# Kernel optimization log

Measured on AMD Instinct MI355X. Metric: run time of the kernel, lower is better.

Reference implementation:

```python
import jax, jax.numpy as jnp
import numpy as np

N, E, DIN, H, D = 100000, 1600000, 256, 4, 32  # nodes, edges, in_feats, heads, out_feats
NEG_SLOPE = 0.2


def setup_inputs() -> dict:
    key = jax.random.key(0)
    ks = jax.random.split(key, 6)
    feat = jax.random.normal(ks[0], (N, DIN), jnp.float32)
    src = jax.random.randint(ks[1], (E,), 0, N, jnp.int32)
    dst = jax.random.randint(ks[2], (E,), 0, N, jnp.int32)
    # fc weight, xavier-normal-ish scale
    W = jax.random.normal(ks[3], (H * D, DIN), jnp.float32) * (2.0 / (DIN + H * D)) ** 0.5
    attn_l = jax.random.normal(ks[4], (1, H, D), jnp.float32) * 0.1
    attn_r = jax.random.normal(ks[5], (1, H, D), jnp.float32) * 0.1
    bias = jnp.zeros((H * D,), jnp.float32)
    return dict(feat=feat, src=src, dst=dst, W=W, attn_l=attn_l, attn_r=attn_r, bias=bias)


def reference(feat, src, dst, W, attn_l, attn_r, bias):
    n = feat.shape[0]
    # node projection: [N, H, D]
    ft = (feat @ W.T).reshape(n, H, D)
    # per-node attention logits: [N, H]
    el = jnp.sum(ft * attn_l, axis=-1)
    er = jnp.sum(ft * attn_r, axis=-1)
    # edge scores (u_add_v + LeakyReLU): [E, H]
    e = jax.nn.leaky_relu(el[src] + er[dst], NEG_SLOPE)
    # segment softmax over incoming edges of each dst node
    m = jax.ops.segment_max(e, dst, num_segments=n)
    m = jnp.where(jnp.isfinite(m), m, 0.0)  # guard zero-in-degree nodes
    ae = jnp.exp(e - m[dst])
    denom = jax.ops.segment_sum(ae, dst, num_segments=n)
    a = ae / denom[dst]  # [E, H]
    # weighted scatter-aggregate (u_mul_e + sum): [N, H, D]
    out = jax.ops.segment_sum(ft[src] * a[:, :, None], dst, num_segments=n)
    return out + bias.reshape(1, H, D)
```

## Files before the change

### kernel.cpp

```cpp
#include <hip/hip_runtime.h>
#include <hip/hip_bf16.h>


#define DIN 256
#define HD 128
#define NEG_SLOPE 0.2f
#define BUCKW 1024
#define BINE 4096
#define CAP  18432

typedef float f32x4 __attribute__((ext_vector_type(4)));
typedef short s16x8 __attribute__((ext_vector_type(8)));

static __device__ __forceinline__ unsigned short f2bf(float x) {
    unsigned u = __float_as_uint(x);
    unsigned r = (u + 0x7FFFu + ((u >> 16) & 1u)) >> 16;
    return (unsigned short)r;
}
static __device__ __forceinline__ uint pk2(float a, float b) {
    return (uint)f2bf(a) | ((uint)f2bf(b) << 16);
}

__global__ void transw_kernel(const float* __restrict__ W, unsigned short* __restrict__ Wtb) {
    int idx = blockIdx.x * blockDim.x + threadIdx.x;
    if (idx >= HD * DIN) return;
    int i = idx & 7, c = (idx >> 3) & 127, kb = idx >> 10;
    Wtb[idx] = f2bf(W[(size_t)c * DIN + kb * 8 + i]);
}

__global__ __launch_bounds__(256, 4) void gemm_kernel(
    const float* __restrict__ feat, const unsigned short* __restrict__ Wtb,
    unsigned short* __restrict__ ftu, const float* __restrict__ attn_l,
    const float* __restrict__ attn_r, float* __restrict__ el,
    float* __restrict__ er, int n)
{
    const int tid = threadIdx.x;
    const int lane = tid & 63;
    const int wv = tid >> 6;
    const int l16 = lane & 15, lq = lane >> 4;
    const int row0 = (int)blockIdx.x * 128 + wv * 32;

    f32x4 acc[2][8] = {};
    const int ar0 = row0 + l16, ar1 = row0 + 16 + l16;
    const bool ok0 = ar0 < n, ok1 = ar1 < n;
    const float* fp0 = feat + (size_t)ar0 * DIN;
    const float* fp1 = feat + (size_t)ar1 * DIN;
#pragma unroll
    for (int kc = 0; kc < 4; ++kc) {
#pragma unroll
        for (int kk = 0; kk < 2; ++kk) {
            const int koff = kc * 64 + kk * 32 + lq * 8;
            union { s16x8 v; uint w[4]; } a0, a1;
            a0.v = (s16x8)(short)0;
            a1.v = (s16x8)(short)0;
            if (ok0) {
                float4 fa = *(const float4*)(fp0 + koff);
                float4 fb = *(const float4*)(fp0 + koff + 4);
                a0.w[0] = pk2(fa.x, fa.y); a0.w[1] = pk2(fa.z, fa.w);
                a0.w[2] = pk2(fb.x, fb.y); a0.w[3] = pk2(fb.z, fb.w);
            }
            if (ok1) {
                float4 fa = *(const float4*)(fp1 + koff);
                float4 fb = *(const float4*)(fp1 + koff + 4);
                a1.w[0] = pk2(fa.x, fa.y); a1.w[1] = pk2(fa.z, fa.w);
                a1.w[2] = pk2(fb.x, fb.y); a1.w[3] = pk2(fb.z, fb.w);
            }
            const int kb = kc * 8 + kk * 4 + lq;
            const unsigned short* bp = Wtb + ((size_t)kb * 128 + l16) * 8;
#pragma unroll
            for (int n4 = 0; n4 < 8; ++n4) {
                s16x8 b = *(const s16x8*)(bp + n4 * 128);
                acc[0][n4] = __builtin_amdgcn_mfma_f32_16x16x32_bf16(a0.v, b, acc[0][n4], 0, 0, 0);
                acc[1][n4] = __builtin_amdgcn_mfma_f32_16x16x32_bf16(a1.v, b, acc[1][n4], 0, 0, 0);
            }
        }
    }

    float al8[8], ar8[8];
#pragma unroll
    for (int n4 = 0; n4 < 8; ++n4) {
        al8[n4] = attn_l[n4 * 16 + l16];
        ar8[n4] = attn_r[n4 * 16 + l16];
    }
#pragma unroll
    for (int m = 0; m < 2; ++m) {
#pragma unroll
        for (int n4 = 0; n4 < 8; ++n4)
#pragma unroll
            for (int j = 0; j < 4; ++j) {
                int r = row0 + m * 16 + lq * 4 + j;
                if (r < n) ftu[(size_t)r * HD + n4 * 16 + l16] = f2bf(acc[m][n4][j]);
            }
#pragma unroll
        for (int j = 0; j < 4; ++j) {
            const int r = row0 + m * 16 + lq * 4 + j;
#pragma unroll
            for (int h = 0; h < 4; ++h) {
                float sl = acc[m][2 * h][j] * al8[2 * h] + acc[m][2 * h + 1][j] * al8[2 * h + 1];
                float sr = acc[m][2 * h][j] * ar8[2 * h] + acc[m][2 * h + 1][j] * ar8[2 * h + 1];
#pragma unroll
                for (int off = 1; off < 16; off <<= 1) {
                    sl += __shfl_xor(sl, off);
                    sr += __shfl_xor(sr, off);
                }
                if (l16 == ((j << 2) | h) && r < n) {
                    el[r * 4 + h] = sl;
                    er[r * 4 + h] = sr;
                }
            }
        }
    }
}

__global__ __launch_bounds__(512) void bin_kernel(
    const int* __restrict__ src, const int* __restrict__ dst,
    int* __restrict__ gcur, int* __restrict__ esrc,
    unsigned short* __restrict__ edlo, int e)
{
    __shared__ int h[128], lb[128], gb[128], sc[128];
    __shared__ int tot;
    __shared__ int ps[BINE];
    __shared__ unsigned short pd[BINE];
    __shared__ unsigned char pb[BINE];
    const int tid = threadIdx.x;
    if (tid < 128) h[tid] = 0;
    __syncthreads();
    const int base = blockIdx.x * BINE + tid * 8;
    int sv[8], dv[8], rk[8];
    const int cnt = min(8, max(0, e - base));
    if (cnt == 8) {
        *(int4*)&sv[0] = *(const int4*)&src[base];
        *(int4*)&sv[4] = *(const int4*)&src[base + 4];
        *(int4*)&dv[0] = *(const int4*)&dst[base];
        *(int4*)&dv[4] = *(const int4*)&dst[base + 4];
    } else {
        for (int m = 0; m < cnt; ++m) { sv[m] = src[base + m]; dv[m] = dst[base + m]; }
    }
    for (int m = 0; m < cnt; ++m)
        rk[m] = atomicAdd(&h[dv[m] >> 10], 1);
    __syncthreads();
    if (tid < 128) sc[tid] = h[tid];
    __syncthreads();
    for (int off = 1; off < 128; off <<= 1) {
        int v = (tid < 128 && tid >= off) ? sc[tid - off] : 0;
        __syncthreads();
        if (tid < 128) sc[tid] += v;
        __syncthreads();
    }
    if (tid < 128) {
        lb[tid] = sc[tid] - h[tid];
        if (h[tid] > 0) gb[tid] = atomicAdd(&gcur[tid], h[tid]);
    }
    if (tid == 127) tot = sc[127];
    __syncthreads();
    for (int m = 0; m < cnt; ++m) {
        int b = dv[m] >> 10;
        int pos = lb[b] + rk[m];
        ps[pos] = sv[m];
        pd[pos] = (unsigned short)(dv[m] & 1023);
        pb[pos] = (unsigned char)b;
    }
    __syncthreads();
    for (int s = tid; s < tot; s += 512) {
        int b = pb[s];
        int o = b * CAP + gb[b] + (s - lb[b]);
        esrc[o] = ps[s];
        edlo[o] = pd[s];
    }
}

__global__ __launch_bounds__(1024) void fine_kernel(
    const int* __restrict__ esrc, const unsigned short* __restrict__ edlo,
    const int* __restrict__ gcur, int* __restrict__ beg, int* __restrict__ endp,
    int* __restrict__ srcs_sorted, int n)
{
    __shared__ int deg[1024];
    __shared__ int wsum[16];
    const int b = blockIdx.x, tid = threadIdx.x;
    const int lane = tid & 63, wid = tid >> 6;
    const int lo = b * CAP;
    const int cnt = gcur[b];
    const int nbase = b << 10;
    deg[tid] = 0;
    __syncthreads();
    for (int i = tid; i < cnt; i += 1024)
        atomicAdd(&deg[edlo[lo + i]], 1);
    __syncthreads();
    const int d = deg[tid];
    int x = d;
#pragma unroll
    for (int off = 1; off < 64; off <<= 1) {
        int y = __shfl(x, lane - off);
        if (lane >= off) x += y;
    }
    if (lane == 63) wsum[wid] = x;
    __syncthreads();
    if (tid == 0) {
        int run = 0;
#pragma unroll
        for (int i2 = 0; i2 < 16; ++i2) { int t2 = wsum[i2]; wsum[i2] = run; run += t2; }
    }
    __syncthreads();
    const int start = lo + wsum[wid] + x - d;
    if (nbase + tid < n) {
        beg[nbase + tid] = start;
        endp[nbase + tid] = start + d;
    }
    deg[tid] = start;
    __syncthreads();
    for (int i = tid; i < cnt; i += 1024) {
        int dd = edlo[lo + i];
        int pos = atomicAdd(&deg[dd], 1);
        srcs_sorted[pos] = esrc[lo + i];
    }
}

__global__ __launch_bounds__(256) void aggregate_kernel(
    const unsigned short* __restrict__ ftu, const float* __restrict__ el,
    const float* __restrict__ er, const int* __restrict__ beg,
    const int* __restrict__ endp, const int* __restrict__ srcs,
    const float* __restrict__ bias, float* __restrict__ out, int n)
{
    __shared__ float plds[4][64][4];
    int v = (int)((blockIdx.x * (unsigned)blockDim.x + threadIdx.x) >> 6);
    if (v >= n) return;
    const int wv = (threadIdx.x >> 6) & 3;
    const int lane = threadIdx.x & 63;
    const int h = lane >> 4;
    const int beg_ = beg[v], end_ = endp[v];
    const float4 er4 = *(const float4*)(er + (size_t)v * 4);
    const uint* __restrict__ ftu32 = (const uint*)ftu;
    float* pl = &plds[wv][0][0];
    float dn = 0.f;
    float acc0 = 0.f, acc1 = 0.f;
    for (int t = beg_; t < end_; t += 64) {
        const int cnt = min(64, end_ - t);
        int sj = 0;
        float p0 = 0.f, p1 = 0.f, p2 = 0.f, p3 = 0.f;
        if (lane < cnt) {
            sj = srcs[t + lane];
            float4 elv = *(const float4*)(el + (size_t)sj * 4);
            float e0 = elv.x + er4.x, e1 = elv.y + er4.y;
            float e2 = elv.z + er4.z, e3 = elv.w + er4.w;
            e0 = fmaxf(e0, NEG_SLOPE * e0);
            e1 = fmaxf(e1, NEG_SLOPE * e1);
            e2 = fmaxf(e2, NEG_SLOPE * e2);
            e3 = fmaxf(e3, NEG_SLOPE * e3);
            p0 = __expf(e0); p1 = __expf(e1);
            p2 = __expf(e2); p3 = __expf(e3);
        }
        *(float4*)&pl[lane << 2] = make_float4(p0, p1, p2, p3);
        __builtin_amdgcn_wave_barrier();
        for (int j = 0; j < cnt; j += 16) {
            uint u[16];
            float pj[16];
#pragma unroll
            for (int m = 0; m < 16; ++m) {
                int sjb = __shfl(sj, j + m);
                u[m] = ftu32[(uint)sjb * 64u + (uint)lane];
                pj[m] = pl[((j + m) << 2) + h];
            }
#pragma unroll
            for (int m = 0; m < 16; ++m) {
                dn += pj[m];
                acc0 = fmaf(pj[m], __uint_as_float(u[m] << 16), acc0);
                acc1 = fmaf(pj[m], __uint_as_float(u[m] & 0xffff0000u), acc1);
            }
        }
        __builtin_amdgcn_wave_barrier();
    }
    float inv = dn > 0.f ? 1.f / dn : 0.f;
    float b0 = bias[lane << 1], b1 = bias[(lane << 1) + 1];
    float2 o = make_float2(fmaf(acc0, inv, b0), fmaf(acc1, inv, b1));
    *(float2*)&out[(size_t)v * HD + (lane << 1)] = o;
}

extern "C" void kernel_launch(void* const* d_in, const int* in_sizes, int n_in,
                              void* d_out, int out_size, void* d_ws, size_t ws_size,
                              hipStream_t stream) {
    const float* feat   = (const float*)d_in[0];
    const int*   src    = (const int*)d_in[1];
    const int*   dst    = (const int*)d_in[2];
    const float* W      = (const float*)d_in[3];
    const float* attn_l = (const float*)d_in[4];
    const float* attn_r = (const float*)d_in[5];
    const float* bias   = (const float*)d_in[6];
    float* out = (float*)d_out;
    const int N = in_sizes[0] / DIN;
    const int E = in_sizes[1];
    const int NBUCK = (N + BUCKW - 1) / BUCKW;
    const int NGB = (N + 127) / 128;
    const int EB = (E + BINE - 1) / BINE;

    char* w = (char*)d_ws;
    auto alloc = [&](size_t bytes) {
        char* p = w;
        w += (bytes + 255) & ~(size_t)255;
        return p;
    };
    unsigned short* Wtb         = (unsigned short*)alloc((size_t)DIN * HD * 2);
    unsigned short* ftu         = (unsigned short*)alloc((size_t)N * HD * 2);
    float*          el          = (float*)alloc((size_t)N * 4 * 4);
    float*          er          = (float*)alloc((size_t)N * 4 * 4);
    int*            beg         = (int*)alloc((size_t)N * 4);
    int*            endp        = (int*)alloc((size_t)N * 4);
    int*            srcs_sorted = (int*)alloc((size_t)NBUCK * CAP * 4);
    int*            esrc        = (int*)alloc((size_t)NBUCK * CAP * 4);
    unsigned short* edlo        = (unsigned short*)alloc((size_t)NBUCK * CAP * 2);
    int*            gcur        = (int*)alloc(128 * 4);
    (void)ws_size;

    hipMemsetAsync(gcur, 0, 128 * 4, stream);
    transw_kernel<<<(HD * DIN + 255) / 256, 256, 0, stream>>>(W, Wtb);
    gemm_kernel<<<NGB, 256, 0, stream>>>(feat, Wtb, ftu, attn_l, attn_r, el, er, N);
    bin_kernel<<<EB, 512, 0, stream>>>(src, dst, gcur, esrc, edlo, E);
    fine_kernel<<<NBUCK, 1024, 0, stream>>>(esrc, edlo, gcur, beg, endp, srcs_sorted, N);
    aggregate_kernel<<<(N + 3) / 4, 256, 0, stream>>>(ftu, el, er, beg, endp, srcs_sorted, bias, out, N);
}
```

Measured before the change: 166.4 us.

## Merge independent kernels into heterogeneous launches and pre-convert features to bf16

Replaces five launches with three. Transposing W, converting feat to bf16 and edge binning now share one grid, and the GEMM shares a grid with the fine per-bucket sort, with blockIdx ranges picking the role. The GEMM now reads a bf16 copy of feat and uses 512-thread blocks with one 16-row tile per wave, while fine sort runs with 512 threads handling two nodes each. The aim is to cut launch gaps and let independent stages overlap, but it adds an extra full pass writing and re-reading a 51 MB bf16 feature buffer.

```diff
diff --git a/kernel.cpp b/kernel.cpp
--- a/kernel.cpp
+++ b/kernel.cpp
@@ -21,101 +21,12 @@
     return (uint)f2bf(a) | ((uint)f2bf(b) << 16);
 }
 
-__global__ void transw_kernel(const float* __restrict__ W, unsigned short* __restrict__ Wtb) {
-    int idx = blockIdx.x * blockDim.x + threadIdx.x;
-    if (idx >= HD * DIN) return;
-    int i = idx & 7, c = (idx >> 3) & 127, kb = idx >> 10;
-    Wtb[idx] = f2bf(W[(size_t)c * DIN + kb * 8 + i]);
-}
-
-__global__ __launch_bounds__(256, 4) void gemm_kernel(
-    const float* __restrict__ feat, const unsigned short* __restrict__ Wtb,
-    unsigned short* __restrict__ ftu, const float* __restrict__ attn_l,
-    const float* __restrict__ attn_r, float* __restrict__ el,
-    float* __restrict__ er, int n)
-{
-    const int tid = threadIdx.x;
-    const int lane = tid & 63;
-    const int wv = tid >> 6;
-    const int l16 = lane & 15, lq = lane >> 4;
-    const int row0 = (int)blockIdx.x * 128 + wv * 32;
-
-    f32x4 acc[2][8] = {};
-    const int ar0 = row0 + l16, ar1 = row0 + 16 + l16;
-    const bool ok0 = ar0 < n, ok1 = ar1 < n;
-    const float* fp0 = feat + (size_t)ar0 * DIN;
-    const float* fp1 = feat + (size_t)ar1 * DIN;
-#pragma unroll
-    for (int kc = 0; kc < 4; ++kc) {
-#pragma unroll
-        for (int kk = 0; kk < 2; ++kk) {
-            const int koff = kc * 64 + kk * 32 + lq * 8;
-            union { s16x8 v; uint w[4]; } a0, a1;
-            a0.v = (s16x8)(short)0;
-            a1.v = (s16x8)(short)0;
-            if (ok0) {
-                float4 fa = *(const float4*)(fp0 + koff);
-                float4 fb = *(const float4*)(fp0 + koff + 4);
-                a0.w[0] = pk2(fa.x, fa.y); a0.w[1] = pk2(fa.z, fa.w);
-                a0.w[2] = pk2(fb.x, fb.y); a0.w[3] = pk2(fb.z, fb.w);
-            }
-            if (ok1) {
-                float4 fa = *(const float4*)(fp1 + koff);
-                float4 fb = *(const float4*)(fp1 + koff + 4);
-                a1.w[0] = pk2(fa.x, fa.y); a1.w[1] = pk2(fa.z, fa.w);
-                a1.w[2] = pk2(fb.x, fb.y); a1.w[3] = pk2(fb.z, fb.w);
-            }
-            const int kb = kc * 8 + kk * 4 + lq;
-            const unsigned short* bp = Wtb + ((size_t)kb * 128 + l16) * 8;
-#pragma unroll
-            for (int n4 = 0; n4 < 8; ++n4) {
-                s16x8 b = *(const s16x8*)(bp + n4 * 128);
-                acc[0][n4] = __builtin_amdgcn_mfma_f32_16x16x32_bf16(a0.v, b, acc[0][n4], 0, 0, 0);
-                acc[1][n4] = __builtin_amdgcn_mfma_f32_16x16x32_bf16(a1.v, b, acc[1][n4], 0, 0, 0);
-            }
-        }
-    }
-
-    float al8[8], ar8[8];
-#pragma unroll
-    for (int n4 = 0; n4 < 8; ++n4) {
-        al8[n4] = attn_l[n4 * 16 + l16];
-        ar8[n4] = attn_r[n4 * 16 + l16];
-    }
-#pragma unroll
-    for (int m = 0; m < 2; ++m) {
-#pragma unroll
-        for (int n4 = 0; n4 < 8; ++n4)
-#pragma unroll
-            for (int j = 0; j < 4; ++j) {
-                int r = row0 + m * 16 + lq * 4 + j;
-                if (r < n) ftu[(size_t)r * HD + n4 * 16 + l16] = f2bf(acc[m][n4][j]);
-            }
-#pragma unroll
-        for (int j = 0; j < 4; ++j) {
-            const int r = row0 + m * 16 + lq * 4 + j;
-#pragma unroll
-            for (int h = 0; h < 4; ++h) {
-                float sl = acc[m][2 * h][j] * al8[2 * h] + acc[m][2 * h + 1][j] * al8[2 * h + 1];
-                float sr = acc[m][2 * h][j] * ar8[2 * h] + acc[m][2 * h + 1][j] * ar8[2 * h + 1];
-#pragma unroll
-                for (int off = 1; off < 16; off <<= 1) {
-                    sl += __shfl_xor(sl, off);
-                    sr += __shfl_xor(sr, off);
-                }
-                if (l16 == ((j << 2) | h) && r < n) {
-                    el[r * 4 + h] = sl;
-                    er[r * 4 + h] = sr;
-                }
-            }
-        }
-    }
-}
-
-__global__ __launch_bounds__(512) void bin_kernel(
+__global__ __launch_bounds__(512) void prep_kernel(
+    const float* __restrict__ feat, unsigned short* __restrict__ featb,
+    const float* __restrict__ W, unsigned short* __restrict__ Wtb,
     const int* __restrict__ src, const int* __restrict__ dst,
     int* __restrict__ gcur, int* __restrict__ esrc,
-    unsigned short* __restrict__ edlo, int e)
+    unsigned short* __restrict__ edlo, long total8, int e, int fb)
 {
     __shared__ int h[128], lb[128], gb[128], sc[128];
     __shared__ int tot;
@@ -123,9 +34,32 @@
     __shared__ unsigned short pd[BINE];
     __shared__ unsigned char pb[BINE];
     const int tid = threadIdx.x;
+    const int bx = (int)blockIdx.x;
+
+    if (bx < fb) {
+        long e8 = (long)bx * 512 + tid;
+        if (e8 < total8) {
+            const float* fp = feat + e8 * 8;
+            float4 a = *(const float4*)fp;
+            float4 b = *(const float4*)(fp + 4);
+            uint4 pk;
+            pk.x = pk2(a.x, a.y); pk.y = pk2(a.z, a.w);
+            pk.z = pk2(b.x, b.y); pk.w = pk2(b.z, b.w);
+            *(uint4*)&featb[e8 * 8] = pk;
+        }
+        return;
+    }
+    if (bx == fb) {
+        for (int idx = tid; idx < HD * DIN; idx += 512) {
+            int i = idx & 7, c = (idx >> 3) & 127, kb = idx >> 10;
+            Wtb[idx] = f2bf(W[(size_t)c * DIN + kb * 8 + i]);
+        }
+        return;
+    }
+
     if (tid < 128) h[tid] = 0;
     __syncthreads();
-    const int base = blockIdx.x * BINE + tid * 8;
+    const int base = (bx - fb - 1) * BINE + tid * 8;
     int sv[8], dv[8], rk[8];
     const int cnt = min(8, max(0, e - base));
     if (cnt == 8) {
@@ -169,49 +103,123 @@
     }
 }
 
-__global__ __launch_bounds__(1024) void fine_kernel(
+__global__ __launch_bounds__(512, 5) void gemm_fine_kernel(
+    const unsigned short* __restrict__ featb, const unsigned short* __restrict__ Wtb,
+    unsigned short* __restrict__ ftu, const float* __restrict__ attn_l,
+    const float* __restrict__ attn_r, float* __restrict__ el,
+    float* __restrict__ er, int n,
     const int* __restrict__ esrc, const unsigned short* __restrict__ edlo,
     const int* __restrict__ gcur, int* __restrict__ beg, int* __restrict__ endp,
-    int* __restrict__ srcs_sorted, int n)
+    int* __restrict__ srcs_sorted, int ngb)
 {
     __shared__ int deg[1024];
-    __shared__ int wsum[16];
-    const int b = blockIdx.x, tid = threadIdx.x;
-    const int lane = tid & 63, wid = tid >> 6;
-    const int lo = b * CAP;
-    const int cnt = gcur[b];
-    const int nbase = b << 10;
-    deg[tid] = 0;
-    __syncthreads();
-    for (int i = tid; i < cnt; i += 1024)
-        atomicAdd(&deg[edlo[lo + i]], 1);
-    __syncthreads();
-    const int d = deg[tid];
-    int x = d;
-#pragma unroll
-    for (int off = 1; off < 64; off <<= 1) {
-        int y = __shfl(x, lane - off);
-        if (lane >= off) x += y;
-    }
-    if (lane == 63) wsum[wid] = x;
-    __syncthreads();
-    if (tid == 0) {
-        int run = 0;
-#pragma unroll
-        for (int i2 = 0; i2 < 16; ++i2) { int t2 = wsum[i2]; wsum[i2] = run; run += t2; }
-    }
-    __syncthreads();
-    const int start = lo + wsum[wid] + x - d;
-    if (nbase + tid < n) {
-        beg[nbase + tid] = start;
-        endp[nbase + tid] = start + d;
-    }
-    deg[tid] = start;
-    __syncthreads();
-    for (int i = tid; i < cnt; i += 1024) {
-        int dd = edlo[lo + i];
-        int pos = atomicAdd(&deg[dd], 1);
-        srcs_sorted[pos] = esrc[lo + i];
+    __shared__ int wsum[8];
+    const int tid = threadIdx.x;
+
+    if ((int)blockIdx.x >= ngb) {
+        const int b = (int)blockIdx.x - ngb;
+        const int lane = tid & 63, wid = tid >> 6;
+        const int lo = b * CAP;
+        const int cnt = gcur[b];
+        const int nbase = b << 10;
+        deg[tid] = 0;
+        deg[tid + 512] = 0;
+        __syncthreads();
+        for (int i = tid; i < cnt; i += 512)
+            atomicAdd(&deg[edlo[lo + i]], 1);
+        __syncthreads();
+        const int d0 = deg[2 * tid], d1 = deg[2 * tid + 1];
+        const int s = d0 + d1;
+        int x = s;
+#pragma unroll
+        for (int off = 1; off < 64; off <<= 1) {
+            int y = __shfl(x, lane - off);
+            if (lane >= off) x += y;
+        }
+        if (lane == 63) wsum[wid] = x;
+        __syncthreads();
+        if (tid == 0) {
+            int run = 0;
+#pragma unroll
+            for (int i2 = 0; i2 < 8; ++i2) { int t2 = wsum[i2]; wsum[i2] = run; run += t2; }
+        }
+        __syncthreads();
+        const int start0 = lo + wsum[wid] + x - s;
+        const int start1 = start0 + d0;
+        if (nbase + 2 * tid < n) {
+            beg[nbase + 2 * tid] = start0;
+            endp[nbase + 2 * tid] = start0 + d0;
+        }
+        if (nbase + 2 * tid + 1 < n) {
+            beg[nbase + 2 * tid + 1] = start1;
+            endp[nbase + 2 * tid + 1] = start1 + d1;
+        }
+        deg[2 * tid] = start0;
+        deg[2 * tid + 1] = start1;
+        __syncthreads();
+        for (int i = tid; i < cnt; i += 512) {
+            int dd = edlo[lo + i];
+            int pos = atomicAdd(&deg[dd], 1);
+            srcs_sorted[pos] = esrc[lo + i];
+        }
+        return;
+    }
+
+    const int lane = tid & 63;
+    const int wv = tid >> 6;
+    const int l16 = lane & 15, lq = lane >> 4;
+    const int row0 = (int)blockIdx.x * 128 + wv * 16;
+    const int arow = row0 + l16;
+    const bool ok = arow < n;
+    const unsigned short* fp = featb + (size_t)arow * DIN;
+
+    f32x4 acc[8] = {};
+#pragma unroll
+    for (int kc = 0; kc < 4; ++kc) {
+#pragma unroll
+        for (int kk = 0; kk < 2; ++kk) {
+            s16x8 a = (s16x8)(short)0;
+            if (ok) a = *(const s16x8*)(fp + kc * 64 + kk * 32 + lq * 8);
+            const int kb = kc * 8 + kk * 4 + lq;
+            const unsigned short* bp = Wtb + ((size_t)kb * 128 + l16) * 8;
+#pragma unroll
+            for (int n4 = 0; n4 < 8; ++n4) {
+                s16x8 b = *(const s16x8*)(bp + n4 * 128);
+                acc[n4] = __builtin_amdgcn_mfma_f32_16x16x32_bf16(a, b, acc[n4], 0, 0, 0);
+            }
+        }
+    }
+
+    float al8[8], ar8[8];
+#pragma unroll
+    for (int n4 = 0; n4 < 8; ++n4) {
+        al8[n4] = attn_l[n4 * 16 + l16];
+        ar8[n4] = attn_r[n4 * 16 + l16];
+    }
+#pragma unroll
+    for (int n4 = 0; n4 < 8; ++n4)
+#pragma unroll
+        for (int j = 0; j < 4; ++j) {
+            int r = row0 + lq * 4 + j;
+            if (r < n) ftu[(size_t)r * HD + n4 * 16 + l16] = f2bf(acc[n4][j]);
+        }
+#pragma unroll
+    for (int j = 0; j < 4; ++j) {
+        const int r = row0 + lq * 4 + j;
+#pragma unroll
+        for (int h = 0; h < 4; ++h) {
+            float sl = acc[2 * h][j] * al8[2 * h] + acc[2 * h + 1][j] * al8[2 * h + 1];
+            float sr = acc[2 * h][j] * ar8[2 * h] + acc[2 * h + 1][j] * ar8[2 * h + 1];
+#pragma unroll
+            for (int off = 1; off < 16; off <<= 1) {
+                sl += __shfl_xor(sl, off);
+                sr += __shfl_xor(sr, off);
+            }
+            if (l16 == ((j << 2) | h) && r < n) {
+                el[r * 4 + h] = sl;
+                er[r * 4 + h] = sr;
+            }
+        }
     }
 }
 
@@ -291,6 +299,8 @@
     const int NBUCK = (N + BUCKW - 1) / BUCKW;
     const int NGB = (N + 127) / 128;
     const int EB = (E + BINE - 1) / BINE;
+    const long TOTAL8 = (long)N * DIN / 8;
+    const int FB = (int)((TOTAL8 + 511) / 512);
 
     char* w = (char*)d_ws;
     auto alloc = [&](size_t bytes) {
@@ -298,6 +308,7 @@
         w += (bytes + 255) & ~(size_t)255;
         return p;
     };
+    unsigned short* featb       = (unsigned short*)alloc((size_t)N * DIN * 2);
     unsigned short* Wtb         = (unsigned short*)alloc((size_t)DIN * HD * 2);
     unsigned short* ftu         = (unsigned short*)alloc((size_t)N * HD * 2);
     float*          el          = (float*)alloc((size_t)N * 4 * 4);
@@ -311,9 +322,11 @@
     (void)ws_size;
 
     hipMemsetAsync(gcur, 0, 128 * 4, stream);
-    transw_kernel<<<(HD * DIN + 255) / 256, 256, 0, stream>>>(W, Wtb);
-    gemm_kernel<<<NGB, 256, 0, stream>>>(feat, Wtb, ftu, attn_l, attn_r, el, er, N);
-    bin_kernel<<<EB, 512, 0, stream>>>(src, dst, gcur, esrc, edlo, E);
-    fine_kernel<<<NBUCK, 1024, 0, stream>>>(esrc, edlo, gcur, beg, endp, srcs_sorted, N);
-    aggregate_kernel<<<(N + 3) / 4, 256, 0, stream>>>(ftu, el, er, beg, endp, srcs_sorted, bias, out, N);
-}
+    prep_kernel<<<FB + 1 + EB, 512, 0, stream>>>(
+        feat, featb, W, Wtb, src, dst, gcur, esrc, edlo, TOTAL8, E, FB);
+    gemm_fine_kernel<<<NGB + NBUCK, 512, 0, stream>>>(
+        featb, Wtb, ftu, attn_l, attn_r, el, er, N,
+        esrc, edlo, gcur, beg, endp, srcs_sorted, NGB);
+    aggregate_kernel<<<(N + 3) / 4, 256, 0, stream>>>(
+        ftu, el, er, beg, endp, srcs_sorted, bias, out, N);
+}
```

Result: slower. 184.0 us (+10.6%).

## Merge GEMM and edge-binning into one launch with block-range dispatch

Applied to the files above, without the earlier changes.

Combines the node-projection GEMM and the edge bucketing kernel into a single launch, where the first NGB blocks run the GEMM and the rest do binning, so the two independent phases can run concurrently on the GPU. The GEMM is reshaped to 512 threads with each wave handling 16 rows instead of 32, which keeps the per-block row count the same but halves the register accumulators per wave. The conversion to bf16 now uses the library intrinsic. The trade-off is that the GEMM blocks must carry the binning kernel's large shared-memory footprint, which can reduce occupancy, and the smaller per-wave tiles reuse B-fragment loads less.

```diff
diff --git a/kernel.cpp b/kernel.cpp
--- a/kernel.cpp
+++ b/kernel.cpp
@@ -17,105 +17,24 @@
     unsigned r = (u + 0x7FFFu + ((u >> 16) & 1u)) >> 16;
     return (unsigned short)r;
 }
-static __device__ __forceinline__ uint pk2(float a, float b) {
-    return (uint)f2bf(a) | ((uint)f2bf(b) << 16);
-}
-
-__global__ void transw_kernel(const float* __restrict__ W, unsigned short* __restrict__ Wtb) {
+
+__global__ __launch_bounds__(512) void transw_kernel(
+    const float* __restrict__ W, unsigned short* __restrict__ Wtb)
+{
     int idx = blockIdx.x * blockDim.x + threadIdx.x;
     if (idx >= HD * DIN) return;
     int i = idx & 7, c = (idx >> 3) & 127, kb = idx >> 10;
     Wtb[idx] = f2bf(W[(size_t)c * DIN + kb * 8 + i]);
 }
 
-__global__ __launch_bounds__(256, 4) void gemm_kernel(
+__global__ __launch_bounds__(512, 4) void gemm_bin_kernel(
     const float* __restrict__ feat, const unsigned short* __restrict__ Wtb,
     unsigned short* __restrict__ ftu, const float* __restrict__ attn_l,
     const float* __restrict__ attn_r, float* __restrict__ el,
-    float* __restrict__ er, int n)
-{
-    const int tid = threadIdx.x;
-    const int lane = tid & 63;
-    const int wv = tid >> 6;
-    const int l16 = lane & 15, lq = lane >> 4;
-    const int row0 = (int)blockIdx.x * 128 + wv * 32;
-
-    f32x4 acc[2][8] = {};
-    const int ar0 = row0 + l16, ar1 = row0 + 16 + l16;
-    const bool ok0 = ar0 < n, ok1 = ar1 < n;
-    const float* fp0 = feat + (size_t)ar0 * DIN;
-    const float* fp1 = feat + (size_t)ar1 * DIN;
-#pragma unroll
-    for (int kc = 0; kc < 4; ++kc) {
-#pragma unroll
-        for (int kk = 0; kk < 2; ++kk) {
-            const int koff = kc * 64 + kk * 32 + lq * 8;
-            union { s16x8 v; uint w[4]; } a0, a1;
-            a0.v = (s16x8)(short)0;
-            a1.v = (s16x8)(short)0;
-            if (ok0) {
-                float4 fa = *(const float4*)(fp0 + koff);
-                float4 fb = *(const float4*)(fp0 + koff + 4);
-                a0.w[0] = pk2(fa.x, fa.y); a0.w[1] = pk2(fa.z, fa.w);
-                a0.w[2] = pk2(fb.x, fb.y); a0.w[3] = pk2(fb.z, fb.w);
-            }
-            if (ok1) {
-                float4 fa = *(const float4*)(fp1 + koff);
-                float4 fb = *(const float4*)(fp1 + koff + 4);
-                a1.w[0] = pk2(fa.x, fa.y); a1.w[1] = pk2(fa.z, fa.w);
-                a1.w[2] = pk2(fb.x, fb.y); a1.w[3] = pk2(fb.z, fb.w);
-            }
-            const int kb = kc * 8 + kk * 4 + lq;
-            const unsigned short* bp = Wtb + ((size_t)kb * 128 + l16) * 8;
-#pragma unroll
-            for (int n4 = 0; n4 < 8; ++n4) {
-                s16x8 b = *(const s16x8*)(bp + n4 * 128);
-                acc[0][n4] = __builtin_amdgcn_mfma_f32_16x16x32_bf16(a0.v, b, acc[0][n4], 0, 0, 0);
-                acc[1][n4] = __builtin_amdgcn_mfma_f32_16x16x32_bf16(a1.v, b, acc[1][n4], 0, 0, 0);
-            }
-        }
-    }
-
-    float al8[8], ar8[8];
-#pragma unroll
-    for (int n4 = 0; n4 < 8; ++n4) {
-        al8[n4] = attn_l[n4 * 16 + l16];
-        ar8[n4] = attn_r[n4 * 16 + l16];
-    }
-#pragma unroll
-    for (int m = 0; m < 2; ++m) {
-#pragma unroll
-        for (int n4 = 0; n4 < 8; ++n4)
-#pragma unroll
-            for (int j = 0; j < 4; ++j) {
-                int r = row0 + m * 16 + lq * 4 + j;
-                if (r < n) ftu[(size_t)r * HD + n4 * 16 + l16] = f2bf(acc[m][n4][j]);
-            }
-#pragma unroll
-        for (int j = 0; j < 4; ++j) {
-            const int r = row0 + m * 16 + lq * 4 + j;
-#pragma unroll
-            for (int h = 0; h < 4; ++h) {
-                float sl = acc[m][2 * h][j] * al8[2 * h] + acc[m][2 * h + 1][j] * al8[2 * h + 1];
-                float sr = acc[m][2 * h][j] * ar8[2 * h] + acc[m][2 * h + 1][j] * ar8[2 * h + 1];
-#pragma unroll
-                for (int off = 1; off < 16; off <<= 1) {
-                    sl += __shfl_xor(sl, off);
-                    sr += __shfl_xor(sr, off);
-                }
-                if (l16 == ((j << 2) | h) && r < n) {
-                    el[r * 4 + h] = sl;
-                    er[r * 4 + h] = sr;
-                }
-            }
-        }
-    }
-}
-
-__global__ __launch_bounds__(512) void bin_kernel(
+    float* __restrict__ er, int n,
     const int* __restrict__ src, const int* __restrict__ dst,
     int* __restrict__ gcur, int* __restrict__ esrc,
-    unsigned short* __restrict__ edlo, int e)
+    unsigned short* __restrict__ edlo, int e, int ngb)
 {
     __shared__ int h[128], lb[128], gb[128], sc[128];
     __shared__ int tot;
@@ -123,49 +42,123 @@
     __shared__ unsigned short pd[BINE];
     __shared__ unsigned char pb[BINE];
     const int tid = threadIdx.x;
-    if (tid < 128) h[tid] = 0;
-    __syncthreads();
-    const int base = blockIdx.x * BINE + tid * 8;
-    int sv[8], dv[8], rk[8];
-    const int cnt = min(8, max(0, e - base));
-    if (cnt == 8) {
-        *(int4*)&sv[0] = *(const int4*)&src[base];
-        *(int4*)&sv[4] = *(const int4*)&src[base + 4];
-        *(int4*)&dv[0] = *(const int4*)&dst[base];
-        *(int4*)&dv[4] = *(const int4*)&dst[base + 4];
-    } else {
-        for (int m = 0; m < cnt; ++m) { sv[m] = src[base + m]; dv[m] = dst[base + m]; }
-    }
-    for (int m = 0; m < cnt; ++m)
-        rk[m] = atomicAdd(&h[dv[m] >> 10], 1);
-    __syncthreads();
-    if (tid < 128) sc[tid] = h[tid];
-    __syncthreads();
-    for (int off = 1; off < 128; off <<= 1) {
-        int v = (tid < 128 && tid >= off) ? sc[tid - off] : 0;
-        __syncthreads();
-        if (tid < 128) sc[tid] += v;
-        __syncthreads();
-    }
-    if (tid < 128) {
-        lb[tid] = sc[tid] - h[tid];
-        if (h[tid] > 0) gb[tid] = atomicAdd(&gcur[tid], h[tid]);
-    }
-    if (tid == 127) tot = sc[127];
-    __syncthreads();
-    for (int m = 0; m < cnt; ++m) {
-        int b = dv[m] >> 10;
-        int pos = lb[b] + rk[m];
-        ps[pos] = sv[m];
-        pd[pos] = (unsigned short)(dv[m] & 1023);
-        pb[pos] = (unsigned char)b;
-    }
-    __syncthreads();
-    for (int s = tid; s < tot; s += 512) {
-        int b = pb[s];
-        int o = b * CAP + gb[b] + (s - lb[b]);
-        esrc[o] = ps[s];
-        edlo[o] = pd[s];
+
+    if ((int)blockIdx.x >= ngb) {
+        if (tid < 128) h[tid] = 0;
+        __syncthreads();
+        const int base = ((int)blockIdx.x - ngb) * BINE + tid * 8;
+        int sv[8], dv[8], rk[8];
+        const int cnt = min(8, max(0, e - base));
+        if (cnt == 8) {
+            *(int4*)&sv[0] = *(const int4*)&src[base];
+            *(int4*)&sv[4] = *(const int4*)&src[base + 4];
+            *(int4*)&dv[0] = *(const int4*)&dst[base];
+            *(int4*)&dv[4] = *(const int4*)&dst[base + 4];
+        } else {
+            for (int m = 0; m < cnt; ++m) { sv[m] = src[base + m]; dv[m] = dst[base + m]; }
+        }
+        for (int m = 0; m < cnt; ++m)
+            rk[m] = atomicAdd(&h[dv[m] >> 10], 1);
+        __syncthreads();
+        if (tid < 128) sc[tid] = h[tid];
+        __syncthreads();
+        for (int off = 1; off < 128; off <<= 1) {
+            int v = (tid < 128 && tid >= off) ? sc[tid - off] : 0;
+            __syncthreads();
+            if (tid < 128) sc[tid] += v;
+            __syncthreads();
+        }
+        if (tid < 128) {
+            lb[tid] = sc[tid] - h[tid];
+            if (h[tid] > 0) gb[tid] = atomicAdd(&gcur[tid], h[tid]);
+        }
+        if (tid == 127) tot = sc[127];
+        __syncthreads();
+        for (int m = 0; m < cnt; ++m) {
+            int b = dv[m] >> 10;
+            int pos = lb[b] + rk[m];
+            ps[pos] = sv[m];
+            pd[pos] = (unsigned short)(dv[m] & 1023);
+            pb[pos] = (unsigned char)b;
+        }
+        __syncthreads();
+        for (int s = tid; s < tot; s += 512) {
+            int b = pb[s];
+            int o = b * CAP + gb[b] + (s - lb[b]);
+            esrc[o] = ps[s];
+            edlo[o] = pd[s];
+        }
+        return;
+    }
+
+    const int lane = tid & 63;
+    const int wv = tid >> 6;
+    const int l16 = lane & 15, lq = lane >> 4;
+    const int row0 = (int)blockIdx.x * 128 + wv * 16;
+    const int arow = row0 + l16;
+    const bool ok = arow < n;
+    const float* fp = feat + (size_t)arow * DIN;
+
+    f32x4 acc[8] = {};
+#pragma unroll
+    for (int kc = 0; kc < 4; ++kc) {
+#pragma unroll
+        for (int kk = 0; kk < 2; ++kk) {
+            const int koff = kc * 64 + kk * 32 + lq * 8;
+            union { s16x8 v; __hip_bfloat16 bh[8]; } a;
+            a.v = (s16x8)(short)0;
+            if (ok) {
+                float4 fa = *(const float4*)(fp + koff);
+                float4 fb = *(const float4*)(fp + koff + 4);
+                a.bh[0] = __float2bfloat16(fa.x);
+                a.bh[1] = __float2bfloat16(fa.y);
+                a.bh[2] = __float2bfloat16(fa.z);
+                a.bh[3] = __float2bfloat16(fa.w);
+                a.bh[4] = __float2bfloat16(fb.x);
+                a.bh[5] = __float2bfloat16(fb.y);
+                a.bh[6] = __float2bfloat16(fb.z);
+                a.bh[7] = __float2bfloat16(fb.w);
+            }
+            const int kb = kc * 8 + kk * 4 + lq;
+            const unsigned short* bp = Wtb + ((size_t)kb * 128 + l16) * 8;
+#pragma unroll
+            for (int n4 = 0; n4 < 8; ++n4) {
+                s16x8 b = *(const s16x8*)(bp + n4 * 128);
+                acc[n4] = __builtin_amdgcn_mfma_f32_16x16x32_bf16(a.v, b, acc[n4], 0, 0, 0);
+            }
+        }
+    }
+
+    float al8[8], ar8[8];
+#pragma unroll
+    for (int n4 = 0; n4 < 8; ++n4) {
+        al8[n4] = attn_l[n4 * 16 + l16];
+        ar8[n4] = attn_r[n4 * 16 + l16];
+    }
+#pragma unroll
+    for (int n4 = 0; n4 < 8; ++n4)
+#pragma unroll
+        for (int j = 0; j < 4; ++j) {
+            int r = row0 + lq * 4 + j;
+            if (r < n) ftu[(size_t)r * HD + n4 * 16 + l16] = f2bf(acc[n4][j]);
+        }
+#pragma unroll
+    for (int j = 0; j < 4; ++j) {
+        const int r = row0 + lq * 4 + j;
+#pragma unroll
+        for (int hh = 0; hh < 4; ++hh) {
+            float sl = acc[2 * hh][j] * al8[2 * hh] + acc[2 * hh + 1][j] * al8[2 * hh + 1];
+            float sr = acc[2 * hh][j] * ar8[2 * hh] + acc[2 * hh + 1][j] * ar8[2 * hh + 1];
+#pragma unroll
+            for (int off = 1; off < 16; off <<= 1) {
+                sl += __shfl_xor(sl, off);
+                sr += __shfl_xor(sr, off);
+            }
+            if (l16 == ((j << 2) | hh) && r < n) {
+                el[r * 4 + hh] = sl;
+                er[r * 4 + hh] = sr;
+            }
+        }
     }
 }
 
@@ -311,9 +304,11 @@
     (void)ws_size;
 
     hipMemsetAsync(gcur, 0, 128 * 4, stream);
-    transw_kernel<<<(HD * DIN + 255) / 256, 256, 0, stream>>>(W, Wtb);
-    gemm_kernel<<<NGB, 256, 0, stream>>>(feat, Wtb, ftu, attn_l, attn_r, el, er, N);
-    bin_kernel<<<EB, 512, 0, stream>>>(src, dst, gcur, esrc, edlo, E);
+    transw_kernel<<<(HD * DIN + 511) / 512, 512, 0, stream>>>(W, Wtb);
+    gemm_bin_kernel<<<NGB + EB, 512, 0, stream>>>(
+        feat, Wtb, ftu, attn_l, attn_r, el, er, N,
+        src, dst, gcur, esrc, edlo, E, NGB);
     fine_kernel<<<NBUCK, 1024, 0, stream>>>(esrc, edlo, gcur, beg, endp, srcs_sorted, N);
-    aggregate_kernel<<<(N + 3) / 4, 256, 0, stream>>>(ftu, el, er, beg, endp, srcs_sorted, bias, out, N);
-}
+    aggregate_kernel<<<(N + 3) / 4, 256, 0, stream>>>(
+        ftu, el, er, beg, endp, srcs_sorted, bias, out, N);
+}
```

After: 158.8 us. 1.05x faster.
